# Performance work log

Measured on AMD Instinct MI355X. Metric: run time of the kernel, lower is better.

Reference implementation:

```python
import jax, jax.numpy as jnp
import numpy as np

MARGIN = 0.5


def _pairwise_dist(x):
    # Euclidean cdist via ||a||^2 + ||b||^2 - 2ab, with safe sqrt.
    sq = jnp.sum(x * x, axis=-1)  # (N,)
    d2 = sq[:, None] + sq[None, :] - 2.0 * (x @ x.T)
    d2 = jnp.maximum(d2, 0.0)
    return jnp.sqrt(jnp.where(d2 > 0.0, d2, 1.0)) * (d2 > 0.0)


def setup_inputs() -> dict:
    key = jax.random.key(0)
    k1, k2 = jax.random.split(key)
    N, D = 8192, 128
    embeddings = jax.random.normal(k1, (N, D), dtype=jnp.float32)
    labels = jax.random.randint(k2, (N,), 0, 7, dtype=jnp.int64)
    return {"embeddings": embeddings, "labels": labels}


def reference(embeddings, labels):
    N = embeddings.shape[0]
    dist = _pairwise_dist(embeddings)  # (N, N)
    same = labels[:, None] == labels[None, :]
    eye = jnp.eye(N, dtype=bool)
    pos_mask = same & ~eye
    neg_mask = ~same
    big = jnp.asarray(jnp.finfo(dist.dtype).max, dist.dtype)
    # hardest positive: max dist among same-label (excl. self)
    pos_dist = jnp.max(jnp.where(pos_mask, dist, -big), axis=1)
    # hardest negative: min dist among different-label
    neg_dist = jnp.min(jnp.where(neg_mask, dist, big), axis=1)
    valid = jnp.any(pos_mask, axis=1) & jnp.any(neg_mask, axis=1)
    per_row = jax.nn.relu(pos_dist - neg_dist + MARGIN)
    loss_sum = jnp.sum(jnp.where(valid, per_row, 0.0))
    count = jnp.sum(valid)
    return loss_sum / jnp.maximum(count, 1).astype(loss_sum.dtype)
```

## Files before the change

kernel.cpp:

```cpp
#include <hip/hip_runtime.h>

#define N 8192
#define D 128
#define MARGIN 0.5f
#define FLT_BIG 3.402823466e+38f

typedef __bf16 bf16x8 __attribute__((ext_vector_type(8)));
typedef float f32x4 __attribute__((ext_vector_type(4)));

__device__ __forceinline__ unsigned short f2bf_rne(float f) {
  unsigned u = __float_as_uint(f);
  u += 0x7FFFu + ((u >> 16) & 1u);
  return (unsigned short)(u >> 16);
}

__global__ void k_prep(const float* __restrict__ x, const int* __restrict__ lab,
                       unsigned short* __restrict__ xb, float* __restrict__ sq,
                       unsigned* __restrict__ posw, unsigned* __restrict__ negw,
                       unsigned* __restrict__ hist, float* __restrict__ acc,
                       unsigned* __restrict__ ticket) {
  const int t = threadIdx.x;
  const int row = blockIdx.x * 8 + (t >> 5);
  const int l32 = t & 31;
  const float4 v = ((const float4*)x)[row * 32 + l32];
  ushort4 o;
  o.x = f2bf_rne(v.x); o.y = f2bf_rne(v.y);
  o.z = f2bf_rne(v.z); o.w = f2bf_rne(v.w);
  ((ushort4*)xb)[row * 32 + l32] = o;
  float s = v.x * v.x + v.y * v.y + v.z * v.z + v.w * v.w;
#pragma unroll
  for (int off = 1; off < 32; off <<= 1) s += __shfl_xor(s, off, 64);
  if (l32 == 0) {
    sq[row] = s;
    posw[row] = 0u;
    negw[row] = 0x7F800000u;
  }

  if (blockIdx.x == 0) {
    __shared__ unsigned h[8];
    if (t < 8) h[t] = 0u;
    __syncthreads();
    unsigned long long cA = 0ull, cB = 0ull;
#pragma unroll
    for (int it = 0; it < 32; ++it) {
      const int l = lab[t + it * 256] & 7;
      if (l < 4) cA += 1ull << (l * 16);
      else       cB += 1ull << ((l - 4) * 16);
    }
#pragma unroll
    for (int off = 1; off < 64; off <<= 1) {
      cA += __shfl_xor(cA, off, 64);
      cB += __shfl_xor(cB, off, 64);
    }
    if ((t & 63) == 0) {
#pragma unroll
      for (int q = 0; q < 4; ++q) {
        atomicAdd(&h[q],     (unsigned)((cA >> (q * 16)) & 0xFFFFu));
        atomicAdd(&h[4 + q], (unsigned)((cB >> (q * 16)) & 0xFFFFu));
      }
    }
    __syncthreads();
    if (t < 8) hist[t] = h[t];
    if (t == 0) { acc[0] = 0.f; acc[1] = 0.f; ticket[0] = 0u; }
  }
}

__global__ __launch_bounds__(256, 4) void k_mine(
    const unsigned short* __restrict__ xb, const float* __restrict__ sq,
    const int* __restrict__ lab, unsigned* __restrict__ posw, unsigned* __restrict__ negw) {
  __shared__ __align__(16) unsigned short lds_b[64 * 128];
  __shared__ float lds_sq[64];
  __shared__ int lds_lab[64];

  const int t = threadIdx.x;
  const int w = t >> 6;
  const int lane = t & 63;
  const int col = lane & 15;
  const int quad = lane >> 4;
  const int iblk = blockIdx.x * 128;
  const int i0 = iblk + w * 32;

  bf16x8 a[2][4];
#pragma unroll
  for (int is = 0; is < 2; ++is) {
    const unsigned short* arow = xb + (size_t)(i0 + is * 16 + col) * D + quad * 8;
#pragma unroll
    for (int k = 0; k < 4; ++k) a[is][k] = *(const bf16x8*)(arow + k * 32);
  }

  int labi[2][4];
#pragma unroll
  for (int is = 0; is < 2; ++is)
#pragma unroll
    for (int r = 0; r < 4; ++r) labi[is][r] = lab[i0 + is * 16 + quad * 4 + r];

  float pos[2][4], neg[2][4];
#pragma unroll
  for (int is = 0; is < 2; ++is)
#pragma unroll
    for (int r = 0; r < 4; ++r) { pos[is][r] = -FLT_BIG; neg[is][r] = FLT_BIG; }

  const int cm = col & 7;
  int coff[4];
#pragma unroll
  for (int k = 0; k < 4; ++k) coff[k] = col * 256 + (((k * 4 + quad) ^ cm) * 16);

  const int jbase = blockIdx.y * 512;
  for (int jt = 0; jt < 8; ++jt) {
    const int j0 = jbase + jt * 64;
    __syncthreads();
#pragma unroll
    for (int p = 0; p < 4; ++p) {
      const int row = p * 16 + (t >> 4);
      const int cg = t & 15;
      const uint4 v = *(const uint4*)(xb + (size_t)(j0 + row) * D + cg * 8);
      *(uint4*)((char*)lds_b + row * 256 + ((cg ^ (row & 7)) * 16)) = v;
    }
    if (t < 64) { lds_sq[t] = sq[j0 + t]; lds_lab[t] = lab[j0 + t]; }
    __syncthreads();

    const bool diag = (j0 < iblk + 128) && (iblk < j0 + 64);

#pragma unroll
    for (int s = 0; s < 4; ++s) {
      f32x4 acc0 = {0.f, 0.f, 0.f, 0.f}, acc1 = {0.f, 0.f, 0.f, 0.f};
#pragma unroll
      for (int k = 0; k < 4; ++k) {
        const bf16x8 b = *(const bf16x8*)((const char*)lds_b + s * 4096 + coff[k]);
        acc0 = __builtin_amdgcn_mfma_f32_16x16x32_bf16(a[0][k], b, acc0, 0, 0, 0);
        acc1 = __builtin_amdgcn_mfma_f32_16x16x32_bf16(a[1][k], b, acc1, 0, 0, 0);
      }
      const int jc = s * 16 + col;
      const float sqj = lds_sq[jc];
      const int labj = lds_lab[jc];
      if (!diag) {
#pragma unroll
        for (int r = 0; r < 4; ++r) {
          const float m0 = fmaf(-2.f, acc0[r], sqj);
          const float m1 = fmaf(-2.f, acc1[r], sqj);
          const bool s0 = (labi[0][r] == labj);
          const bool s1 = (labi[1][r] == labj);
          pos[0][r] = fmaxf(pos[0][r], s0 ? m0 : -FLT_BIG);
          neg[0][r] = fminf(neg[0][r], s0 ? FLT_BIG : m0);
          pos[1][r] = fmaxf(pos[1][r], s1 ? m1 : -FLT_BIG);
          neg[1][r] = fminf(neg[1][r], s1 ? FLT_BIG : m1);
        }
      } else {
        const int jg = j0 + jc;
#pragma unroll
        for (int r = 0; r < 4; ++r) {
          const int ir = quad * 4 + r;
          const float m0 = fmaf(-2.f, acc0[r], sqj);
          const float m1 = fmaf(-2.f, acc1[r], sqj);
          const bool s0 = (labi[0][r] == labj) && (jg != i0 + ir);
          const bool s1 = (labi[1][r] == labj) && (jg != i0 + 16 + ir);
          pos[0][r] = fmaxf(pos[0][r], s0 ? m0 : -FLT_BIG);
          neg[0][r] = fminf(neg[0][r], (labi[0][r] == labj) ? FLT_BIG : m0);
          pos[1][r] = fmaxf(pos[1][r], s1 ? m1 : -FLT_BIG);
          neg[1][r] = fminf(neg[1][r], (labi[1][r] == labj) ? FLT_BIG : m1);
        }
      }
    }
  }

#pragma unroll
  for (int is = 0; is < 2; ++is)
#pragma unroll
    for (int r = 0; r < 4; ++r) {
      float p = pos[is][r], n = neg[is][r];
#pragma unroll
      for (int off = 1; off < 16; off <<= 1) {
        p = fmaxf(p, __shfl_xor(p, off, 64));
        n = fminf(n, __shfl_xor(n, off, 64));
      }
      if (col == 0) {
        const int i = i0 + is * 16 + quad * 4 + r;
        const float sqi = sq[i];
        atomicMax(posw + i, __float_as_uint(fmaxf(sqi + p, 0.f)));
        atomicMin(negw + i, __float_as_uint(fmaxf(sqi + n, 0.f)));
      }
    }
}

__global__ void k_tail(const unsigned* __restrict__ posw, const unsigned* __restrict__ negw,
                       const int* __restrict__ lab, const unsigned* __restrict__ hist,
                       float* __restrict__ acc, unsigned* __restrict__ ticket,
                       float* __restrict__ out) {
  __shared__ float ls[4], cs[4];
  const int t = threadIdx.x;
  const int i = blockIdx.x * 256 + t;
  const float pd2 = __uint_as_float(posw[i]);
  const float nd2 = __uint_as_float(negw[i]);
  const unsigned cnt = hist[lab[i] & 7];
  const bool valid = (cnt >= 2u) && (cnt < (unsigned)N);
  float loss = 0.f, c = 0.f;
  if (valid) {
    loss = fmaxf(sqrtf(pd2) - sqrtf(fminf(nd2, FLT_BIG)) + MARGIN, 0.f);
    c = 1.f;
  }
#pragma unroll
  for (int off = 1; off < 64; off <<= 1) {
    loss += __shfl_xor(loss, off, 64);
    c += __shfl_xor(c, off, 64);
  }
  const int wv = t >> 6;
  if ((t & 63) == 0) { ls[wv] = loss; cs[wv] = c; }
  __syncthreads();
  if (t == 0) {
    atomicAdd(acc + 0, ls[0] + ls[1] + ls[2] + ls[3]);
    atomicAdd(acc + 1, cs[0] + cs[1] + cs[2] + cs[3]);
    __threadfence();
    const unsigned tk = atomicAdd(ticket, 1u);
    if (tk == 31u) {
      const float lsum = atomicAdd(acc + 0, 0.f);
      const float csum = atomicAdd(acc + 1, 0.f);
      out[0] = lsum / fmaxf(csum, 1.f);
    }
  }
}

extern "C" void kernel_launch(void* const* d_in, const int* in_sizes, int n_in,
                              void* d_out, int out_size, void* d_ws, size_t ws_size,
                              hipStream_t stream) {
  const float* x = (const float*)d_in[0];
  const int* lab = (const int*)d_in[1];
  char* ws = (char*)d_ws;
  unsigned short* xb = (unsigned short*)ws;
  float* sq = (float*)(ws + (size_t)N * D * 2);
  unsigned* posw = (unsigned*)((char*)sq + (size_t)N * 4);
  unsigned* negw = posw + N;
  unsigned* hist = negw + N;
  unsigned* ticket = hist + 8;
  float* acc = (float*)(ticket + 1);
  float* out = (float*)d_out;

  hipLaunchKernelGGL(k_prep, dim3(1024), dim3(256), 0, stream, x, lab, xb, sq,
                     posw, negw, hist, acc, ticket);
  hipLaunchKernelGGL(k_mine, dim3(64, 16), dim3(256), 0, stream, xb, sq, lab, posw, negw);
  hipLaunchKernelGGL(k_tail, dim3(32), dim3(256), 0, stream, posw, negw, lab, hist,
                     acc, ticket, out);
}
```

Before: 107.8 us.

## Double-buffer column tiles with direct global-to-LDS async loads in k_mine

Replaces the single 64-row LDS tile, with its two barriers per step, by two 32-row LDS buffers. The buffers are filled with global_load_lds direct-to-LDS loads, and the next tile is prefetched while the current one feeds the MFMAs. The XOR swizzle moves to the global-address side. Column norms and labels are kept in registers and prefetched, and launch bounds rise to 5 blocks per CU, all to hide global-load latency and cut barrier stalls. The trade-off is a fully unrolled 16-step loop, smaller tiles, and reliance on the compiler placing vmcnt waits before the barrier for the async LDS loads.

```diff
diff --git a/kernel.cpp b/kernel.cpp
--- a/kernel.cpp
+++ b/kernel.cpp
@@ -65,12 +65,10 @@
   }
 }
 
-__global__ __launch_bounds__(256, 4) void k_mine(
+__global__ __launch_bounds__(256, 5) void k_mine(
     const unsigned short* __restrict__ xb, const float* __restrict__ sq,
     const int* __restrict__ lab, unsigned* __restrict__ posw, unsigned* __restrict__ negw) {
-  __shared__ __align__(16) unsigned short lds_b[64 * 128];
-  __shared__ float lds_sq[64];
-  __shared__ int lds_lab[64];
+  __shared__ __align__(16) unsigned short lds_b[2][32 * 128];
 
   const int t = threadIdx.x;
   const int w = t >> 6;
@@ -79,6 +77,27 @@
   const int quad = lane >> 4;
   const int iblk = blockIdx.x * 128;
   const int i0 = iblk + w * 32;
+  const int jbase = blockIdx.y * 512;
+
+  int srow[2], schunk[2];
+#pragma unroll
+  for (int p = 0; p < 2; ++p) {
+    const int s = p * 4 + w;
+    srow[p] = s * 4 + (lane >> 4);
+    schunk[p] = (lane & 15) ^ (srow[p] & 7);
+  }
+
+#define PREFETCH(J0, BUF)                                                      \
+  {                                                                            \
+    _Pragma("unroll")                                                          \
+    for (int p = 0; p < 2; ++p) {                                              \
+      const unsigned short* g = xb + (size_t)((J0) + srow[p]) * D + schunk[p] * 8; \
+      __builtin_amdgcn_global_load_lds(                                        \
+          (const __attribute__((address_space(1))) void*)g,                    \
+          (__attribute__((address_space(3))) void*)(&lds_b[(BUF)][(p * 4 + w) * 512]), \
+          16, 0, 0);                                                           \
+    }                                                                          \
+  }
 
   bf16x8 a[2][4];
 #pragma unroll
@@ -105,34 +124,43 @@
 #pragma unroll
   for (int k = 0; k < 4; ++k) coff[k] = col * 256 + (((k * 4 + quad) ^ cm) * 16);
 
-  const int jbase = blockIdx.y * 512;
-  for (int jt = 0; jt < 8; ++jt) {
-    const int j0 = jbase + jt * 64;
-    __syncthreads();
-#pragma unroll
-    for (int p = 0; p < 4; ++p) {
-      const int row = p * 16 + (t >> 4);
-      const int cg = t & 15;
-      const uint4 v = *(const uint4*)(xb + (size_t)(j0 + row) * D + cg * 8);
-      *(uint4*)((char*)lds_b + row * 256 + ((cg ^ (row & 7)) * 16)) = v;
-    }
-    if (t < 64) { lds_sq[t] = sq[j0 + t]; lds_lab[t] = lab[j0 + t]; }
-    __syncthreads();
-
-    const bool diag = (j0 < iblk + 128) && (iblk < j0 + 64);
-
-#pragma unroll
-    for (int s = 0; s < 4; ++s) {
+  PREFETCH(jbase, 0);
+  float sqc[2];
+  int labc[2];
+#pragma unroll
+  for (int s = 0; s < 2; ++s) {
+    sqc[s] = sq[jbase + s * 16 + col];
+    labc[s] = lab[jbase + s * 16 + col];
+  }
+  __syncthreads();
+
+#pragma unroll
+  for (int jt = 0; jt < 16; ++jt) {
+    const int cur = jt & 1;
+    const int j0 = jbase + jt * 32;
+    float sqn[2];
+    int labn[2];
+    if (jt < 15) {
+      PREFETCH(j0 + 32, cur ^ 1);
+#pragma unroll
+      for (int s = 0; s < 2; ++s) {
+        sqn[s] = sq[j0 + 32 + s * 16 + col];
+        labn[s] = lab[j0 + 32 + s * 16 + col];
+      }
+    }
+    const bool diag = (j0 < iblk + 128) && (iblk < j0 + 32);
+
+#pragma unroll
+    for (int s = 0; s < 2; ++s) {
       f32x4 acc0 = {0.f, 0.f, 0.f, 0.f}, acc1 = {0.f, 0.f, 0.f, 0.f};
 #pragma unroll
       for (int k = 0; k < 4; ++k) {
-        const bf16x8 b = *(const bf16x8*)((const char*)lds_b + s * 4096 + coff[k]);
+        const bf16x8 b = *(const bf16x8*)((const char*)&lds_b[cur][0] + s * 4096 + coff[k]);
         acc0 = __builtin_amdgcn_mfma_f32_16x16x32_bf16(a[0][k], b, acc0, 0, 0, 0);
         acc1 = __builtin_amdgcn_mfma_f32_16x16x32_bf16(a[1][k], b, acc1, 0, 0, 0);
       }
-      const int jc = s * 16 + col;
-      const float sqj = lds_sq[jc];
-      const int labj = lds_lab[jc];
+      const float sqj = sqc[s];
+      const int labj = labc[s];
       if (!diag) {
 #pragma unroll
         for (int r = 0; r < 4; ++r) {
@@ -146,7 +174,7 @@
           neg[1][r] = fminf(neg[1][r], s1 ? FLT_BIG : m1);
         }
       } else {
-        const int jg = j0 + jc;
+        const int jg = j0 + s * 16 + col;
 #pragma unroll
         for (int r = 0; r < 4; ++r) {
           const int ir = quad * 4 + r;
@@ -161,6 +189,11 @@
         }
       }
     }
+    if (jt < 15) {
+#pragma unroll
+      for (int s = 0; s < 2; ++s) { sqc[s] = sqn[s]; labc[s] = labn[s]; }
+      __syncthreads();
+    }
   }
 
 #pragma unroll
@@ -180,6 +213,7 @@
         atomicMin(negw + i, __float_as_uint(fmaxf(sqi + n, 0.f)));
       }
     }
+#undef PREFETCH
 }
 
 __global__ void k_tail(const unsigned* __restrict__ posw, const unsigned* __restrict__ negw,
```

Result: slower. 166.9 us (+54.7%).

## Load B tiles directly from global into registers with double buffering, drop LDS

Applied to the files above, without the earlier changes.

Removes the shared-memory staging of the column tile and its two block barriers per iteration. Each lane now loads its B fragments straight from global memory into registers, double-buffered across 16-column steps. The j-range per block is halved and the grid doubled so there are more blocks. In exchange, the four waves no longer share B loads, so each block reads the same B rows four times from L2/global, and there are twice as many atomics at the end.

```diff
diff --git a/kernel.cpp b/kernel.cpp
--- a/kernel.cpp
+++ b/kernel.cpp
@@ -68,10 +68,6 @@
 __global__ __launch_bounds__(256, 4) void k_mine(
     const unsigned short* __restrict__ xb, const float* __restrict__ sq,
     const int* __restrict__ lab, unsigned* __restrict__ posw, unsigned* __restrict__ negw) {
-  __shared__ __align__(16) unsigned short lds_b[64 * 128];
-  __shared__ float lds_sq[64];
-  __shared__ int lds_lab[64];
-
   const int t = threadIdx.x;
   const int w = t >> 6;
   const int lane = t & 63;
@@ -79,6 +75,7 @@
   const int quad = lane >> 4;
   const int iblk = blockIdx.x * 128;
   const int i0 = iblk + w * 32;
+  const int jbase = blockIdx.y * 256;
 
   bf16x8 a[2][4];
 #pragma unroll
@@ -100,68 +97,68 @@
 #pragma unroll
     for (int r = 0; r < 4; ++r) { pos[is][r] = -FLT_BIG; neg[is][r] = FLT_BIG; }
 
-  const int cm = col & 7;
-  int coff[4];
-#pragma unroll
-  for (int k = 0; k < 4; ++k) coff[k] = col * 256 + (((k * 4 + quad) ^ cm) * 16);
-
-  const int jbase = blockIdx.y * 512;
-  for (int jt = 0; jt < 8; ++jt) {
-    const int j0 = jbase + jt * 64;
-    __syncthreads();
-#pragma unroll
-    for (int p = 0; p < 4; ++p) {
-      const int row = p * 16 + (t >> 4);
-      const int cg = t & 15;
-      const uint4 v = *(const uint4*)(xb + (size_t)(j0 + row) * D + cg * 8);
-      *(uint4*)((char*)lds_b + row * 256 + ((cg ^ (row & 7)) * 16)) = v;
-    }
-    if (t < 64) { lds_sq[t] = sq[j0 + t]; lds_lab[t] = lab[j0 + t]; }
-    __syncthreads();
-
-    const bool diag = (j0 < iblk + 128) && (iblk < j0 + 64);
-
-#pragma unroll
-    for (int s = 0; s < 4; ++s) {
-      f32x4 acc0 = {0.f, 0.f, 0.f, 0.f}, acc1 = {0.f, 0.f, 0.f, 0.f};
-#pragma unroll
-      for (int k = 0; k < 4; ++k) {
-        const bf16x8 b = *(const bf16x8*)((const char*)lds_b + s * 4096 + coff[k]);
-        acc0 = __builtin_amdgcn_mfma_f32_16x16x32_bf16(a[0][k], b, acc0, 0, 0, 0);
-        acc1 = __builtin_amdgcn_mfma_f32_16x16x32_bf16(a[1][k], b, acc1, 0, 0, 0);
-      }
-      const int jc = s * 16 + col;
-      const float sqj = lds_sq[jc];
-      const int labj = lds_lab[jc];
-      if (!diag) {
-#pragma unroll
-        for (int r = 0; r < 4; ++r) {
-          const float m0 = fmaf(-2.f, acc0[r], sqj);
-          const float m1 = fmaf(-2.f, acc1[r], sqj);
-          const bool s0 = (labi[0][r] == labj);
-          const bool s1 = (labi[1][r] == labj);
-          pos[0][r] = fmaxf(pos[0][r], s0 ? m0 : -FLT_BIG);
-          neg[0][r] = fminf(neg[0][r], s0 ? FLT_BIG : m0);
-          pos[1][r] = fmaxf(pos[1][r], s1 ? m1 : -FLT_BIG);
-          neg[1][r] = fminf(neg[1][r], s1 ? FLT_BIG : m1);
-        }
-      } else {
-        const int jg = j0 + jc;
-#pragma unroll
-        for (int r = 0; r < 4; ++r) {
-          const int ir = quad * 4 + r;
-          const float m0 = fmaf(-2.f, acc0[r], sqj);
-          const float m1 = fmaf(-2.f, acc1[r], sqj);
-          const bool s0 = (labi[0][r] == labj) && (jg != i0 + ir);
-          const bool s1 = (labi[1][r] == labj) && (jg != i0 + 16 + ir);
-          pos[0][r] = fmaxf(pos[0][r], s0 ? m0 : -FLT_BIG);
-          neg[0][r] = fminf(neg[0][r], (labi[0][r] == labj) ? FLT_BIG : m0);
-          pos[1][r] = fmaxf(pos[1][r], s1 ? m1 : -FLT_BIG);
-          neg[1][r] = fminf(neg[1][r], (labi[1][r] == labj) ? FLT_BIG : m1);
-        }
-      }
-    }
-  }
+  bf16x8 bn[2][4];
+  float sqn[2];
+  int labn[2];
+
+#define LOADB(JS, P)                                                               \
+  {                                                                                \
+    const unsigned short* g = xb + (size_t)(jbase + (JS) * 16 + col) * D + quad * 8; \
+    bn[P][0] = *(const bf16x8*)(g);                                                \
+    bn[P][1] = *(const bf16x8*)(g + 32);                                           \
+    bn[P][2] = *(const bf16x8*)(g + 64);                                           \
+    bn[P][3] = *(const bf16x8*)(g + 96);                                           \
+    sqn[P] = sq[jbase + (JS) * 16 + col];                                          \
+    labn[P] = lab[jbase + (JS) * 16 + col];                                        \
+  }
+
+  LOADB(0, 0);
+
+#pragma unroll
+  for (int js = 0; js < 16; ++js) {
+    const int p = js & 1;
+    if (js < 15) LOADB(js + 1, p ^ 1);
+
+    f32x4 acc0 = {0.f, 0.f, 0.f, 0.f}, acc1 = {0.f, 0.f, 0.f, 0.f};
+#pragma unroll
+    for (int k = 0; k < 4; ++k) {
+      acc0 = __builtin_amdgcn_mfma_f32_16x16x32_bf16(a[0][k], bn[p][k], acc0, 0, 0, 0);
+      acc1 = __builtin_amdgcn_mfma_f32_16x16x32_bf16(a[1][k], bn[p][k], acc1, 0, 0, 0);
+    }
+    const float sqj = sqn[p];
+    const int labj = labn[p];
+    const int j0s = jbase + js * 16;
+    const bool diag = (j0s < i0 + 32) && (i0 < j0s + 16);
+
+    if (!diag) {
+#pragma unroll
+      for (int r = 0; r < 4; ++r) {
+        const float m0 = fmaf(-2.f, acc0[r], sqj);
+        const float m1 = fmaf(-2.f, acc1[r], sqj);
+        const bool s0 = (labi[0][r] == labj);
+        const bool s1 = (labi[1][r] == labj);
+        pos[0][r] = fmaxf(pos[0][r], s0 ? m0 : -FLT_BIG);
+        neg[0][r] = fminf(neg[0][r], s0 ? FLT_BIG : m0);
+        pos[1][r] = fmaxf(pos[1][r], s1 ? m1 : -FLT_BIG);
+        neg[1][r] = fminf(neg[1][r], s1 ? FLT_BIG : m1);
+      }
+    } else {
+      const int jg = j0s + col;
+#pragma unroll
+      for (int r = 0; r < 4; ++r) {
+        const int ir = quad * 4 + r;
+        const float m0 = fmaf(-2.f, acc0[r], sqj);
+        const float m1 = fmaf(-2.f, acc1[r], sqj);
+        const bool s0 = (labi[0][r] == labj) && (jg != i0 + ir);
+        const bool s1 = (labi[1][r] == labj) && (jg != i0 + 16 + ir);
+        pos[0][r] = fmaxf(pos[0][r], s0 ? m0 : -FLT_BIG);
+        neg[0][r] = fminf(neg[0][r], (labi[0][r] == labj) ? FLT_BIG : m0);
+        pos[1][r] = fmaxf(pos[1][r], s1 ? m1 : -FLT_BIG);
+        neg[1][r] = fminf(neg[1][r], (labi[1][r] == labj) ? FLT_BIG : m1);
+      }
+    }
+  }
+#undef LOADB
 
 #pragma unroll
   for (int is = 0; is < 2; ++is)
@@ -236,7 +233,7 @@
 
   hipLaunchKernelGGL(k_prep, dim3(1024), dim3(256), 0, stream, x, lab, xb, sq,
                      posw, negw, hist, acc, ticket);
-  hipLaunchKernelGGL(k_mine, dim3(64, 16), dim3(256), 0, stream, xb, sq, lab, posw, negw);
+  hipLaunchKernelGGL(k_mine, dim3(64, 32), dim3(256), 0, stream, xb, sq, lab, posw, negw);
   hipLaunchKernelGGL(k_tail, dim3(32), dim3(256), 0, stream, posw, negw, lab, hist,
                      acc, ticket, out);
 }
```

Result: slower. 145.9 us (+35.3%).
